# Kernel tuning notes

Hardware: AMD Instinct MI355X
Metric: run time of the kernel (lower is better)

Reference implementation:

```python
import jax, jax.numpy as jnp
import numpy as np

N = 30000      # total nodes across batch
E = 480000     # edges (before self-loops)
B = 48         # graphs in batch
H = 4          # heads
D = 64         # hidden per head
NIN = 8
NOUT = 128
L = 10
SLOPE = 0.2    # GATConv default negative_slope


def setup_inputs() -> dict:
    key = jax.random.key(0)
    ks = jax.random.split(key, 12)
    s = 0.05
    x = jax.random.normal(ks[0], (N, NIN), jnp.float32)
    edge_index = jax.random.randint(ks[1], (2, E), 0, N, dtype=jnp.int32)
    batch = jnp.sort(jax.random.randint(ks[2], (N,), 0, B, dtype=jnp.int32))
    # layer 0 params (input dim NIN)
    W0 = jax.random.normal(ks[3], (NIN, H * D), jnp.float32) * s
    a_src0 = jax.random.normal(ks[4], (H, D), jnp.float32) * s
    a_dst0 = jax.random.normal(ks[5], (H, D), jnp.float32) * s
    b0 = jnp.zeros((H * D,), jnp.float32)
    # layers 1..L-1 (input dim H*D)
    Ws = jax.random.normal(ks[6], (L - 1, H * D, H * D), jnp.float32) * s
    a_srcs = jax.random.normal(ks[7], (L - 1, H, D), jnp.float32) * s
    a_dsts = jax.random.normal(ks[8], (L - 1, H, D), jnp.float32) * s
    bs = jnp.zeros((L - 1, H * D), jnp.float32)
    # readout head: GELU -> Linear(4*H*D -> NOUT)
    head_W = jax.random.normal(ks[9], (4 * H * D, NOUT), jnp.float32) * s
    head_b = jnp.zeros((NOUT,), jnp.float32)
    return dict(x=x, edge_index=edge_index, batch=batch,
                W0=W0, a_src0=a_src0, a_dst0=a_dst0, b0=b0,
                Ws=Ws, a_srcs=a_srcs, a_dsts=a_dsts, bs=bs,
                head_W=head_W, head_b=head_b)


def _gat_layer(x, W, a_src, a_dst, b, src, dst):
    n = x.shape[0]
    h = (x @ W).reshape(n, H, D)                      # [N,H,D]
    alpha_src = jnp.einsum('nhd,hd->nh', h, a_src)    # [N,H]
    alpha_dst = jnp.einsum('nhd,hd->nh', h, a_dst)
    e = jax.nn.leaky_relu(alpha_src[src] + alpha_dst[dst], SLOPE)  # [Etot,H]
    # segment softmax over destination neighborhoods
    m = jax.ops.segment_max(e, dst, num_segments=n)
    e = jnp.exp(e - m[dst])
    z = jax.ops.segment_sum(e, dst, num_segments=n)
    alpha = e / (z[dst] + 1e-16)                      # [Etot,H]
    msg = h[src] * alpha[:, :, None]                  # [Etot,H,D]
    out = jax.ops.segment_sum(msg, dst, num_segments=n)
    return out.reshape(n, H * D) + b


def reference(x, edge_index, batch, W0, a_src0, a_dst0, b0,
              Ws, a_srcs, a_dsts, bs, head_W, head_b):
    # add self loops (GATConv default add_self_loops=True)
    loops = jnp.arange(N, dtype=edge_index.dtype)
    src = jnp.concatenate([edge_index[0], loops])
    dst = jnp.concatenate([edge_index[1], loops])

    h = _gat_layer(x, W0, a_src0, a_dst0, b0, src, dst)
    for i in range(L - 1):
        h = jax.nn.gelu(h, approximate=False)  # dropout = identity (eval)
        h = _gat_layer(h, Ws[i], a_srcs[i], a_dsts[i], bs[i], src, dst)

    # MultiAggregation([min, max, mean, sum]) over graphs
    cnt = jax.ops.segment_sum(jnp.ones((N,), h.dtype), batch, num_segments=B)
    g_sum = jax.ops.segment_sum(h, batch, num_segments=B)
    g_mean = g_sum / jnp.maximum(cnt, 1.0)[:, None]
    g_min = jax.ops.segment_min(h, batch, num_segments=B)
    g_max = jax.ops.segment_max(h, batch, num_segments=B)
    g = jnp.concatenate([g_min, g_max, g_mean, g_sum], axis=-1)  # [B, 4*H*D]

    return jax.nn.gelu(g, approximate=False) @ head_W + head_b   # [B, NOUT]
```

## Files before the change

kernel.cpp:

```cpp
#include <hip/hip_runtime.h>
#include <math.h>

#define NN   30000
#define EE   480000
#define ETOT 510000
#define BB   48
#define HHH  4
#define DDD  64
#define CCH  256
#define NINP 8
#define NOUTP 128
#define NLAY 10
#define SLOPE 0.2f
#define PCHUNK 32

typedef short v8s  __attribute__((ext_vector_type(8)));
typedef float v4f  __attribute__((ext_vector_type(4)));

__device__ __forceinline__ float gelu_f(float x){
    return 0.5f * x * (1.0f + erff(x * 0.70710678118654752f));
}
__device__ __forceinline__ unsigned short f2bf(float f){
    unsigned u = __float_as_uint(f);
    unsigned r = u + 0x7FFF + ((u >> 16) & 1);
    return (unsigned short)(r >> 16);
}
__device__ __forceinline__ float bf2f(unsigned short b){
    return __uint_as_float(((unsigned)b) << 16);
}
__device__ __forceinline__ float lrelu(float e){
    return (e > 0.f) ? e : SLOPE * e;
}
__device__ __forceinline__ unsigned pack2(float a, float b){
    return (unsigned)f2bf(a) | ((unsigned)f2bf(b) << 16);
}
__device__ __forceinline__ float4 up4(uint2 u){
    float4 r;
    r.x = __uint_as_float(u.x << 16);
    r.y = __uint_as_float(u.x & 0xFFFF0000u);
    r.z = __uint_as_float(u.y << 16);
    r.w = __uint_as_float(u.y & 0xFFFF0000u);
    return r;
}

__global__ void count_k(const int* __restrict__ ei, int* __restrict__ cnt){
    int e = blockIdx.x * 256 + threadIdx.x;
    if (e >= ETOT) return;
    int d = (e < EE) ? ei[EE + e] : (e - EE);
    atomicAdd(&cnt[d], 1);
}

__global__ __launch_bounds__(1024) void scan_k(const int* __restrict__ cnt, int* __restrict__ row_ptr){
    const int PER = 30;
    int t = threadIdx.x;
    int base = t * PER;
    int v[PER];
    int sum = 0;
#pragma unroll
    for (int i = 0; i < PER; ++i){
        int x = (base + i < NN) ? cnt[base + i] : 0;
        v[i] = sum;
        sum += x;
    }
    int lane = t & 63, w = t >> 6;
    int inc = sum;
#pragma unroll
    for (int off = 1; off < 64; off <<= 1){
        int u = __shfl_up(inc, off);
        if (lane >= off) inc += u;
    }
    __shared__ int wtot[16], woff[16];
    if (lane == 63) wtot[w] = inc;
    __syncthreads();
    if (t == 0){
        int r = 0;
        for (int i = 0; i < 16; ++i){ woff[i] = r; r += wtot[i]; }
        row_ptr[NN] = r;
    }
    __syncthreads();
    int excl = woff[w] + (inc - sum);
#pragma unroll
    for (int i = 0; i < PER; ++i){
        if (base + i < NN) row_ptr[base + i] = excl + v[i];
    }
}

__global__ void scatter_k(const int* __restrict__ ei, const int* __restrict__ row_ptr,
                          int* __restrict__ cursor, int* __restrict__ csr_src){
    int e = blockIdx.x * 256 + threadIdx.x;
    if (e >= ETOT) return;
    int s, d;
    if (e < EE){ s = ei[e]; d = ei[EE + e]; } else { s = d = e - EE; }
    int pos = row_ptr[d] + atomicAdd(&cursor[d], 1);
    csr_src[pos] = s;
}

__global__ __launch_bounds__(256) void wconv_k(const float* __restrict__ Ws,
                                               unsigned short* __restrict__ WT_hi,
                                               unsigned short* __restrict__ WT_lo){
    __shared__ float tile[32][33];
    int l = blockIdx.x;
    int kt = (blockIdx.y >> 3) * 32;
    int nt = (blockIdx.y & 7) * 32;
    const float* W = Ws + (size_t)l * CCH * CCH;
    unsigned short* th = WT_hi + (size_t)l * CCH * CCH;
    unsigned short* tl = WT_lo + (size_t)l * CCH * CCH;
    int tx = threadIdx.x & 31, ty = threadIdx.x >> 5;
#pragma unroll
    for (int r = ty; r < 32; r += 8)
        tile[r][tx] = W[(size_t)(kt + r) * CCH + nt + tx];
    __syncthreads();
#pragma unroll
    for (int r = ty; r < 32; r += 8){
        float w = tile[tx][r];
        unsigned short h = f2bf(w);
        size_t o = (size_t)(nt + r) * CCH + kt + tx;
        th[o] = h;
        tl[o] = f2bf(w - bf2f(h));
    }
}

__global__ __launch_bounds__(256) void waconv_k(const float* __restrict__ Ws,
                                                const float* __restrict__ a_srcs,
                                                const float* __restrict__ a_dsts,
                                                unsigned short* __restrict__ wa_hi,
                                                unsigned short* __restrict__ wa_lo){
    int l = blockIdx.x;
    int j = blockIdx.y;
    int k = threadIdx.x;
    const float* W = Ws + (size_t)l * CCH * CCH;
    const float* av = (j < 4) ? (a_srcs + (size_t)l * CCH + j * DDD)
                              : (a_dsts + (size_t)l * CCH + (j - 4) * DDD);
    int cb = (j & 3) * DDD;
    float s = 0.f;
    const float4* wp = (const float4*)(W + (size_t)k * CCH + cb);
    const float4* ap = (const float4*)av;
#pragma unroll
    for (int d = 0; d < DDD / 4; ++d){
        float4 wv = wp[d], avv = ap[d];
        s += wv.x * avv.x + wv.y * avv.y + wv.z * avv.z + wv.w * avv.w;
    }
    unsigned short hb = f2bf(s);
    wa_hi[((size_t)l * 16 + j) * CCH + k] = hb;
    wa_lo[((size_t)l * 16 + j) * CCH + k] = f2bf(s - bf2f(hb));
    if (j >= 4){
        wa_hi[((size_t)l * 16 + j + 4) * CCH + k] = 0;
        wa_lo[((size_t)l * 16 + j + 4) * CCH + k] = 0;
        wa_hi[((size_t)l * 16 + j + 8) * CCH + k] = 0;
        wa_lo[((size_t)l * 16 + j + 8) * CCH + k] = 0;
    }
}

__global__ __launch_bounds__(256) void l0_fused(const float* __restrict__ x,
                                                const float* __restrict__ W0,
                                                const float* __restrict__ a_src,
                                                const float* __restrict__ a_dst,
                                                unsigned short* __restrict__ hout,
                                                float* __restrict__ asb,
                                                float* __restrict__ adb){
    __shared__ float xs[NINP];
    int n = blockIdx.x;
    int c = threadIdx.x;
    if (c < NINP) xs[c] = x[n * NINP + c];
    __syncthreads();
    float acc = 0.f;
#pragma unroll
    for (int k = 0; k < NINP; ++k) acc += xs[k] * W0[k * CCH + c];
    hout[(size_t)n * CCH + c] = f2bf(acc);
    int hh = c >> 6, lane = c & 63;
    float s1 = acc * a_src[hh * DDD + lane];
    float s2 = acc * a_dst[hh * DDD + lane];
#pragma unroll
    for (int off = 32; off; off >>= 1){
        s1 += __shfl_xor(s1, off);
        s2 += __shfl_xor(s2, off);
    }
    if (lane == 0){
        asb[(size_t)n * HHH + hh] = s1;
        adb[(size_t)n * HHH + hh] = s2;
    }
}

__global__ __launch_bounds__(256) void gemm_mfma(const unsigned short* __restrict__ A,
                                                 const unsigned short* __restrict__ Bhi,
                                                 const unsigned short* __restrict__ Blo,
                                                 const unsigned short* __restrict__ WAhi,
                                                 const unsigned short* __restrict__ WAlo,
                                                 unsigned short* __restrict__ C,
                                                 float* __restrict__ asb,
                                                 float* __restrict__ adb){
    int tid  = threadIdx.x;
    int lane = tid & 63, wave = tid >> 6;
    int wr = wave >> 1, wc = wave & 1;
    int rowBase = blockIdx.y * 128 + wr * 64;
    int colBase = blockIdx.x * 128 + wc * 64;
    int fr = lane & 15;
    int kg = lane >> 4;
    bool doAlpha = (blockIdx.x == 0) && (wc == 0);

    v4f acc[4][4];
#pragma unroll
    for (int mi = 0; mi < 4; ++mi)
#pragma unroll
        for (int ni = 0; ni < 4; ++ni) acc[mi][ni] = (v4f){0.f, 0.f, 0.f, 0.f};
    v4f acca[4];
#pragma unroll
    for (int mi = 0; mi < 4; ++mi) acca[mi] = (v4f){0.f, 0.f, 0.f, 0.f};

    const unsigned short* aptr[4];
#pragma unroll
    for (int mi = 0; mi < 4; ++mi){
        int r = rowBase + mi * 16 + fr;
        if (r >= NN) r = NN - 1;
        aptr[mi] = A + (size_t)r * CCH + kg * 8;
    }
    const unsigned short* bhp[4];
    const unsigned short* blp[4];
#pragma unroll
    for (int ni = 0; ni < 4; ++ni){
        int c = colBase + ni * 16 + fr;
        bhp[ni] = Bhi + (size_t)c * CCH + kg * 8;
        blp[ni] = Blo + (size_t)c * CCH + kg * 8;
    }
    const unsigned short* wahp = WAhi + (size_t)fr * CCH + kg * 8;
    const unsigned short* walp = WAlo + (size_t)fr * CCH + kg * 8;

    for (int kc = 0; kc < CCH; kc += 32){
        v8s a[4], bh[4], bl[4];
#pragma unroll
        for (int mi = 0; mi < 4; ++mi) a[mi] = *(const v8s*)(aptr[mi] + kc);
#pragma unroll
        for (int ni = 0; ni < 4; ++ni){
            bh[ni] = *(const v8s*)(bhp[ni] + kc);
            bl[ni] = *(const v8s*)(blp[ni] + kc);
        }
#pragma unroll
        for (int mi = 0; mi < 4; ++mi)
#pragma unroll
            for (int ni = 0; ni < 4; ++ni){
                acc[mi][ni] = __builtin_amdgcn_mfma_f32_16x16x32_bf16(a[mi], bh[ni], acc[mi][ni], 0, 0, 0);
                acc[mi][ni] = __builtin_amdgcn_mfma_f32_16x16x32_bf16(a[mi], bl[ni], acc[mi][ni], 0, 0, 0);
            }
        if (doAlpha){
            v8s wh = *(const v8s*)(wahp + kc);
            v8s wl = *(const v8s*)(walp + kc);
#pragma unroll
            for (int mi = 0; mi < 4; ++mi){
                acca[mi] = __builtin_amdgcn_mfma_f32_16x16x32_bf16(a[mi], wh, acca[mi], 0, 0, 0);
                acca[mi] = __builtin_amdgcn_mfma_f32_16x16x32_bf16(a[mi], wl, acca[mi], 0, 0, 0);
            }
        }
    }

#pragma unroll
    for (int mi = 0; mi < 4; ++mi)
#pragma unroll
        for (int j = 0; j < 4; ++j){
            int r = rowBase + mi * 16 + kg * 4 + j;
            if (r < NN){
#pragma unroll
                for (int ni = 0; ni < 4; ++ni)
                    C[(size_t)r * CCH + colBase + ni * 16 + fr] = f2bf(acc[mi][ni][j]);
            }
        }
    if (doAlpha){
#pragma unroll
        for (int mi = 0; mi < 4; ++mi)
#pragma unroll
            for (int j = 0; j < 4; ++j){
                int r = rowBase + mi * 16 + kg * 4 + j;
                if (r < NN){
                    float val = acca[mi][j];
                    if (fr < 4)      asb[(size_t)r * HHH + fr]       = val;
                    else if (fr < 8) adb[(size_t)r * HHH + (fr - 4)] = val;
                }
            }
    }
}

#define LOADG8(gg, U0, U1, U2, U3, A0, A1, A2, A3)                     \
    { int _b = (gg) << 3;                                              \
      int _e0 = _b + half, _e1 = _b + 2 + half;                        \
      int _e2 = _b + 4 + half, _e3 = _b + 6 + half;                    \
      int _i0 = ix_w[_e0], _i1 = ix_w[_e1];                            \
      int _i2 = ix_w[_e2], _i3 = ix_w[_e3];                            \
      A0 = al_w[_e0 * HHH + hc8];                                      \
      A1 = al_w[_e1 * HHH + hc8];                                      \
      A2 = al_w[_e2 * HHH + hc8];                                      \
      A3 = al_w[_e3 * HHH + hc8];                                      \
      U0 = *(const uint4*)(h + (size_t)_i0 * CCH + coff8);             \
      U1 = *(const uint4*)(h + (size_t)_i1 * CCH + coff8);             \
      U2 = *(const uint4*)(h + (size_t)_i2 * CCH + coff8);             \
      U3 = *(const uint4*)(h + (size_t)_i3 * CCH + coff8); }

#define CONSUME8(U0, U1, U2, U3, A0, A1, A2, A3)                       \
    { float4 _l0 = up4(make_uint2(U0.x, U0.y)), _h0 = up4(make_uint2(U0.z, U0.w)); \
      float4 _l1 = up4(make_uint2(U1.x, U1.y)), _h1 = up4(make_uint2(U1.z, U1.w)); \
      float4 _l2 = up4(make_uint2(U2.x, U2.y)), _h2 = up4(make_uint2(U2.z, U2.w)); \
      float4 _l3 = up4(make_uint2(U3.x, U3.y)), _h3 = up4(make_uint2(U3.z, U3.w)); \
      accLo.x += _l0.x * A0 + _l1.x * A1 + _l2.x * A2 + _l3.x * A3;    \
      accLo.y += _l0.y * A0 + _l1.y * A1 + _l2.y * A2 + _l3.y * A3;    \
      accLo.z += _l0.z * A0 + _l1.z * A1 + _l2.z * A2 + _l3.z * A3;    \
      accLo.w += _l0.w * A0 + _l1.w * A1 + _l2.w * A2 + _l3.w * A3;    \
      accHi.x += _h0.x * A0 + _h1.x * A1 + _h2.x * A2 + _h3.x * A3;    \
      accHi.y += _h0.y * A0 + _h1.y * A1 + _h2.y * A2 + _h3.y * A3;    \
      accHi.z += _h0.z * A0 + _h1.z * A1 + _h2.z * A2 + _h3.z * A3;    \
      accHi.w += _h0.w * A0 + _h1.w * A1 + _h2.w * A2 + _h3.w * A3; }

__global__ __launch_bounds__(256) void agg_k(const unsigned short* __restrict__ h,
                                             const float* __restrict__ asrc,
                                             const float* __restrict__ adst,
                                             const float* __restrict__ bias,
                                             const int* __restrict__ row_ptr,
                                             const int* __restrict__ csr_src,
                                             unsigned short* __restrict__ outg,
                                             float* __restrict__ outf,
                                             int mode){
    __shared__ float s_al[4][64 * HHH];
    __shared__ int   s_ix[4][64];

    int wave = threadIdx.x >> 6, lane = threadIdx.x & 63;
    int n = blockIdx.x * 4 + wave;
    int row0 = row_ptr[n];
    int deg  = row_ptr[n + 1] - row0;
    float4 ad = *(const float4*)(adst + (size_t)n * HHH);
    float* al_w = s_al[wave];
    int*   ix_w = s_ix[wave];

    if (deg <= 64){
        int k = lane;
        int s = 0;
        float e0 = -INFINITY, e1 = -INFINITY, e2 = -INFINITY, e3 = -INFINITY;
        if (k < deg){
            s = csr_src[row0 + k];
            float4 as = *(const float4*)(asrc + (size_t)s * HHH);
            e0 = lrelu(as.x + ad.x); e1 = lrelu(as.y + ad.y);
            e2 = lrelu(as.z + ad.z); e3 = lrelu(as.w + ad.w);
        }
        float m0 = e0, m1 = e1, m2 = e2, m3 = e3;
#pragma unroll
        for (int off = 32; off; off >>= 1){
            m0 = fmaxf(m0, __shfl_xor(m0, off));
            m1 = fmaxf(m1, __shfl_xor(m1, off));
            m2 = fmaxf(m2, __shfl_xor(m2, off));
            m3 = fmaxf(m3, __shfl_xor(m3, off));
        }
        float x0 = 0.f, x1 = 0.f, x2 = 0.f, x3 = 0.f;
        if (k < deg){
            x0 = __expf(e0 - m0); x1 = __expf(e1 - m1);
            x2 = __expf(e2 - m2); x3 = __expf(e3 - m3);
        }
        float z0 = x0, z1 = x1, z2 = x2, z3 = x3;
#pragma unroll
        for (int off = 32; off; off >>= 1){
            z0 += __shfl_xor(z0, off);
            z1 += __shfl_xor(z1, off);
            z2 += __shfl_xor(z2, off);
            z3 += __shfl_xor(z3, off);
        }
        if (k < deg){
            float4 alv;
            alv.x = x0 / (z0 + 1e-16f);
            alv.y = x1 / (z1 + 1e-16f);
            alv.z = x2 / (z2 + 1e-16f);
            alv.w = x3 / (z3 + 1e-16f);
            ix_w[k] = s;
            *(float4*)&al_w[k * HHH] = alv;
        }
        int half  = lane >> 5;
        int l32   = lane & 31;
        int coff8 = l32 << 3;
        int hc8   = l32 >> 3;
        float4 accLo = make_float4(0.f, 0.f, 0.f, 0.f);
        float4 accHi = make_float4(0.f, 0.f, 0.f, 0.f);

        int ng = deg >> 3;
        uint4 uA0, uA1, uA2, uA3, uB0, uB1, uB2, uB3;
        float aA0, aA1, aA2, aA3, aB0, aB1, aB2, aB3;
        if (ng > 0) LOADG8(0, uA0, uA1, uA2, uA3, aA0, aA1, aA2, aA3);
        if (ng > 1) LOADG8(1, uB0, uB1, uB2, uB3, aB0, aB1, aB2, aB3);
        for (int g = 0; g < ng; g += 2){
            if (g + 2 < ng) {
                CONSUME8(uA0, uA1, uA2, uA3, aA0, aA1, aA2, aA3);
                LOADG8(g + 2, uA0, uA1, uA2, uA3, aA0, aA1, aA2, aA3);
            } else {
                CONSUME8(uA0, uA1, uA2, uA3, aA0, aA1, aA2, aA3);
            }
            if (g + 1 < ng){
                if (g + 3 < ng) {
                    CONSUME8(uB0, uB1, uB2, uB3, aB0, aB1, aB2, aB3);
                    LOADG8(g + 3, uB0, uB1, uB2, uB3, aB0, aB1, aB2, aB3);
                } else {
                    CONSUME8(uB0, uB1, uB2, uB3, aB0, aB1, aB2, aB3);
                }
            }
        }
        for (int kk = ng << 3; kk < deg; kk += 2){
            int e = kk + half;
            if (e < deg){
                int i0 = ix_w[e];
                float a0 = al_w[e * HHH + hc8];
                uint4 u = *(const uint4*)(h + (size_t)i0 * CCH + coff8);
                float4 lo = up4(make_uint2(u.x, u.y)), hi = up4(make_uint2(u.z, u.w));
                accLo.x += lo.x * a0; accLo.y += lo.y * a0;
                accLo.z += lo.z * a0; accLo.w += lo.w * a0;
                accHi.x += hi.x * a0; accHi.y += hi.y * a0;
                accHi.z += hi.z * a0; accHi.w += hi.w * a0;
            }
        }
        accLo.x += __shfl_xor(accLo.x, 32); accLo.y += __shfl_xor(accLo.y, 32);
        accLo.z += __shfl_xor(accLo.z, 32); accLo.w += __shfl_xor(accLo.w, 32);
        accHi.x += __shfl_xor(accHi.x, 32); accHi.y += __shfl_xor(accHi.y, 32);
        accHi.z += __shfl_xor(accHi.z, 32); accHi.w += __shfl_xor(accHi.w, 32);
        if (half == 0){
            float4 b0v = *(const float4*)(bias + coff8);
            float4 b1v = *(const float4*)(bias + coff8 + 4);
            accLo.x += b0v.x; accLo.y += b0v.y; accLo.z += b0v.z; accLo.w += b0v.w;
            accHi.x += b1v.x; accHi.y += b1v.y; accHi.z += b1v.z; accHi.w += b1v.w;
            if (mode == 0){
                uint4 o;
                o.x = pack2(gelu_f(accLo.x), gelu_f(accLo.y));
                o.y = pack2(gelu_f(accLo.z), gelu_f(accLo.w));
                o.z = pack2(gelu_f(accHi.x), gelu_f(accHi.y));
                o.w = pack2(gelu_f(accHi.z), gelu_f(accHi.w));
                *(uint4*)(outg + (size_t)n * CCH + coff8) = o;
            } else {
                *(float4*)(outf + (size_t)n * CCH + coff8)     = accLo;
                *(float4*)(outf + (size_t)n * CCH + coff8 + 4) = accHi;
            }
        }
        return;
    }

    int coff = lane << 2;
    int hc   = lane >> 4;
    float4 acc = make_float4(0.f, 0.f, 0.f, 0.f);
    float m0 = -INFINITY, m1 = -INFINITY, m2 = -INFINITY, m3 = -INFINITY;
    float z0 = 0.f, z1 = 0.f, z2 = 0.f, z3 = 0.f;
    for (int c0 = 0; c0 < deg; c0 += 64){
        int k = c0 + lane;
        float e0 = -INFINITY, e1 = -INFINITY, e2 = -INFINITY, e3 = -INFINITY;
        if (k < deg){
            int s = csr_src[row0 + k];
            float4 as = *(const float4*)(asrc + (size_t)s * HHH);
            e0 = lrelu(as.x + ad.x); e1 = lrelu(as.y + ad.y);
            e2 = lrelu(as.z + ad.z); e3 = lrelu(as.w + ad.w);
        }
        float c0m = e0, c1m = e1, c2m = e2, c3m = e3;
#pragma unroll
        for (int off = 32; off; off >>= 1){
            c0m = fmaxf(c0m, __shfl_xor(c0m, off));
            c1m = fmaxf(c1m, __shfl_xor(c1m, off));
            c2m = fmaxf(c2m, __shfl_xor(c2m, off));
            c3m = fmaxf(c3m, __shfl_xor(c3m, off));
        }
        float n0 = fmaxf(m0, c0m), n1 = fmaxf(m1, c1m);
        float n2 = fmaxf(m2, c2m), n3 = fmaxf(m3, c3m);
        float x0 = 0.f, x1 = 0.f, x2 = 0.f, x3 = 0.f;
        if (k < deg){
            x0 = __expf(e0 - n0); x1 = __expf(e1 - n1);
            x2 = __expf(e2 - n2); x3 = __expf(e3 - n3);
        }
        float s0 = x0, s1 = x1, s2 = x2, s3 = x3;
#pragma unroll
        for (int off = 32; off; off >>= 1){
            s0 += __shfl_xor(s0, off);
            s1 += __shfl_xor(s1, off);
            s2 += __shfl_xor(s2, off);
            s3 += __shfl_xor(s3, off);
        }
        z0 = z0 * ((m0 == -INFINITY) ? 0.f : __expf(m0 - n0)) + s0;
        z1 = z1 * ((m1 == -INFINITY) ? 0.f : __expf(m1 - n1)) + s1;
        z2 = z2 * ((m2 == -INFINITY) ? 0.f : __expf(m2 - n2)) + s2;
        z3 = z3 * ((m3 == -INFINITY) ? 0.f : __expf(m3 - n3)) + s3;
        m0 = n0; m1 = n1; m2 = n2; m3 = n3;
    }
    float iz0 = 1.f / (z0 + 1e-16f), iz1 = 1.f / (z1 + 1e-16f);
    float iz2 = 1.f / (z2 + 1e-16f), iz3 = 1.f / (z3 + 1e-16f);
    for (int c0 = 0; c0 < deg; c0 += 64){
        int k = c0 + lane;
        if (k < deg){
            int s = csr_src[row0 + k];
            float4 as = *(const float4*)(asrc + (size_t)s * HHH);
            float4 alv;
            alv.x = __expf(lrelu(as.x + ad.x) - m0) * iz0;
            alv.y = __expf(lrelu(as.y + ad.y) - m1) * iz1;
            alv.z = __expf(lrelu(as.z + ad.z) - m2) * iz2;
            alv.w = __expf(lrelu(as.w + ad.w) - m3) * iz3;
            ix_w[lane] = s;
            *(float4*)&al_w[lane * HHH] = alv;
        }
        int cnt = deg - c0; if (cnt > 64) cnt = 64;
        for (int j = 0; j < cnt; ++j){
            int i0 = ix_w[j];
            float a0 = al_w[j * HHH + hc];
            float4 v0 = up4(*(const uint2*)(h + (size_t)i0 * CCH + coff));
            acc.x += v0.x * a0; acc.y += v0.y * a0; acc.z += v0.z * a0; acc.w += v0.w * a0;
        }
    }
    float4 bv = *(const float4*)(bias + coff);
    acc.x += bv.x; acc.y += bv.y; acc.z += bv.z; acc.w += bv.w;
    if (mode == 0){
        uint2 o;
        o.x = pack2(gelu_f(acc.x), gelu_f(acc.y));
        o.y = pack2(gelu_f(acc.z), gelu_f(acc.w));
        *(uint2*)(outg + (size_t)n * CCH + coff) = o;
    } else {
        *(float4*)(outf + (size_t)n * CCH + coff) = acc;
    }
}

__global__ void gptr_k(const int* __restrict__ batch, int* __restrict__ gptr){
    int i = blockIdx.x * 256 + threadIdx.x;
    if (i >= NN) return;
    int bi = batch[i];
    int bp = (i == 0) ? -1 : batch[i - 1];
    for (int g = bp + 1; g <= bi; ++g) gptr[g] = i;
    if (i == NN - 1){
        for (int g = bi + 1; g <= BB; ++g) gptr[g] = NN;
    }
}

__global__ __launch_bounds__(256) void pool1_k(const float* __restrict__ h,
                                               const int* __restrict__ gptr,
                                               float* __restrict__ part){
    const int S1 = BB * PCHUNK * CCH;
    int b = blockIdx.x, j = blockIdx.y, c = threadIdx.x;
    int s = gptr[b], e = gptr[b + 1];
    int len = e - s;
    int per = (len + PCHUNK - 1) / PCHUNK;
    int r0 = s + j * per;
    int r1 = r0 + per; if (r1 > e) r1 = e;
    float mn = INFINITY, mx = -INFINITY, sm = 0.f;
    int n = r0;
    for (; n + 4 <= r1; n += 4){
        float v0 = h[(size_t)(n + 0) * CCH + c];
        float v1 = h[(size_t)(n + 1) * CCH + c];
        float v2 = h[(size_t)(n + 2) * CCH + c];
        float v3 = h[(size_t)(n + 3) * CCH + c];
        mn = fminf(mn, fminf(fminf(v0, v1), fminf(v2, v3)));
        mx = fmaxf(mx, fmaxf(fmaxf(v0, v1), fmaxf(v2, v3)));
        sm += (v0 + v1) + (v2 + v3);
    }
    for (; n < r1; ++n){
        float v = h[(size_t)n * CCH + c];
        mn = fminf(mn, v); mx = fmaxf(mx, v); sm += v;
    }
    size_t o = ((size_t)b * PCHUNK + j) * CCH + c;
    part[o] = mn; part[S1 + o] = mx; part[2 * (size_t)S1 + o] = sm;
}

__global__ __launch_bounds__(256) void pool2_k(const float* __restrict__ part,
                                               const int* __restrict__ gptr,
                                               float* __restrict__ gbuf){
    const int S1 = BB * PCHUNK * CCH;
    int b = blockIdx.x, c = threadIdx.x;
    float mn = INFINITY, mx = -INFINITY, sm = 0.f;
#pragma unroll
    for (int j = 0; j < PCHUNK; ++j){
        size_t o = ((size_t)b * PCHUNK + j) * CCH + c;
        mn = fminf(mn, part[o]);
        mx = fmaxf(mx, part[S1 + o]);
        sm += part[2 * (size_t)S1 + o];
    }
    int cnt = gptr[b + 1] - gptr[b];
    float mean = sm / fmaxf((float)cnt, 1.0f);
    if (cnt == 0){ mn = 0.f; mx = 0.f; }
    gbuf[b * 4 * CCH + 0 * CCH + c] = mn;
    gbuf[b * 4 * CCH + 1 * CCH + c] = mx;
    gbuf[b * 4 * CCH + 2 * CCH + c] = mean;
    gbuf[b * 4 * CCH + 3 * CCH + c] = sm;
}

__global__ __launch_bounds__(128) void head_k(const float* __restrict__ gbuf,
                                              const float* __restrict__ head_W,
                                              const float* __restrict__ head_b,
                                              float* __restrict__ out){
    __shared__ float gs[4 * CCH];
    int b = blockIdx.x;
    int o = threadIdx.x;
    for (int k = o; k < 4 * CCH; k += 128) gs[k] = gelu_f(gbuf[b * 4 * CCH + k]);
    __syncthreads();
    float acc = head_b[o];
    for (int k = 0; k < 4 * CCH; ++k) acc += gs[k] * head_W[k * NOUTP + o];
    out[b * NOUTP + o] = acc;
}

extern "C" void kernel_launch(void* const* d_in, const int* in_sizes, int n_in,
                              void* d_out, int out_size, void* d_ws, size_t ws_size,
                              hipStream_t stream){
    const float* x        = (const float*)d_in[0];
    const int*   ei       = (const int*)  d_in[1];
    const int*   batch    = (const int*)  d_in[2];
    const float* W0       = (const float*)d_in[3];
    const float* a_src0   = (const float*)d_in[4];
    const float* a_dst0   = (const float*)d_in[5];
    const float* b0       = (const float*)d_in[6];
    const float* Ws       = (const float*)d_in[7];
    const float* a_srcs   = (const float*)d_in[8];
    const float* a_dsts   = (const float*)d_in[9];
    const float* bs       = (const float*)d_in[10];
    const float* head_W   = (const float*)d_in[11];
    const float* head_b   = (const float*)d_in[12];
    float* out = (float*)d_out;

    char* p = (char*)d_ws;
    float* buf0f = (float*)p;                   p += (size_t)NN * CCH * 4;
    unsigned short* buf0g = (unsigned short*)p; p += (size_t)NN * CCH * 2;
    unsigned short* buf1  = (unsigned short*)p; p += (size_t)NN * CCH * 2;
    float* asb  = (float*)p;                   p += (size_t)NN * HHH * 4;
    float* adb  = (float*)p;                   p += (size_t)NN * HHH * 4;
    int* row_ptr = (int*)p;                    p += 120016;
    int* cnt     = (int*)p;                    p += (size_t)NN * 4;
    int* csr_src = (int*)p;                    p += (size_t)ETOT * 4;
    float* gbuf  = (float*)p;                  p += (size_t)BB * 4 * CCH * 4;
    int* gptr    = (int*)p;                    p += 208;
    unsigned short* wthi = (unsigned short*)p; p += (size_t)(NLAY - 1) * CCH * CCH * 2;
    unsigned short* wtlo = (unsigned short*)p; p += (size_t)(NLAY - 1) * CCH * CCH * 2;
    unsigned short* wahi = (unsigned short*)p; p += (size_t)(NLAY - 1) * 16 * CCH * 2;
    unsigned short* walo = (unsigned short*)p; p += (size_t)(NLAY - 1) * 16 * CCH * 2;
    float* pscr = (float*)p;                   p += (size_t)3 * BB * PCHUNK * CCH * 4;

    hipMemsetAsync(cnt, 0, (size_t)NN * 4, stream);
    count_k<<<(ETOT + 255) / 256, 256, 0, stream>>>(ei, cnt);
    scan_k<<<1, 1024, 0, stream>>>(cnt, row_ptr);
    hipMemsetAsync(cnt, 0, (size_t)NN * 4, stream);
    scatter_k<<<(ETOT + 255) / 256, 256, 0, stream>>>(ei, row_ptr, cnt, csr_src);
    gptr_k<<<(NN + 255) / 256, 256, 0, stream>>>(batch, gptr);
    wconv_k<<<dim3(NLAY - 1, 64), 256, 0, stream>>>(Ws, wthi, wtlo);
    waconv_k<<<dim3(NLAY - 1, 8), 256, 0, stream>>>(Ws, a_srcs, a_dsts, wahi, walo);

    l0_fused<<<NN, 256, 0, stream>>>(x, W0, a_src0, a_dst0, buf1, asb, adb);
    agg_k<<<NN / 4, 256, 0, stream>>>(buf1, asb, adb, b0, row_ptr, csr_src,
                                      buf0g, buf0f, 0);

    dim3 ggrid(2, (NN + 127) / 128);
    for (int l = 1; l < NLAY; ++l){
        const unsigned short* whl = wthi + (size_t)(l - 1) * CCH * CCH;
        const unsigned short* wll = wtlo + (size_t)(l - 1) * CCH * CCH;
        const unsigned short* wal_h = wahi + (size_t)(l - 1) * 16 * CCH;
        const unsigned short* wal_l = walo + (size_t)(l - 1) * 16 * CCH;
        const float* bl  = bs + (size_t)(l - 1) * CCH;
        gemm_mfma<<<ggrid, 256, 0, stream>>>(buf0g, whl, wll, wal_h, wal_l, buf1, asb, adb);
        agg_k<<<NN / 4, 256, 0, stream>>>(buf1, asb, adb, bl, row_ptr, csr_src,
                                          buf0g, buf0f, (l == NLAY - 1) ? 1 : 0);
    }

    dim3 pgrid(BB, PCHUNK);
    pool1_k<<<pgrid, 256, 0, stream>>>(buf0f, gptr, pscr);
    pool2_k<<<BB, 256, 0, stream>>>(pscr, gptr, gbuf);
    head_k<<<BB, 128, 0, stream>>>(gbuf, head_W, head_b, out);
}
```

Measured before the change: 979.6 us.

## Aggregate two destination nodes per wave and drop softmax max subtraction

Each wave of the aggregation kernel now processes two destination nodes. It issues the first neighbour-row gathers for both nodes before consuming either, so more independent global loads are in flight to hide gather latency, and the grid is halved accordingly. The segment-softmax max reduction is removed: logits are exponentiated directly, which saves one cross-lane reduction per head. In exchange it risks overflow or precision loss if attention logits become large. If either node has degree above 64, both fall back to the generic per-node path.

```diff
diff --git a/kernel.cpp b/kernel.cpp
--- a/kernel.cpp
+++ b/kernel.cpp
@@ -278,160 +278,14 @@
     }
 }
 
-#define LOADG8(gg, U0, U1, U2, U3, A0, A1, A2, A3)                     \
-    { int _b = (gg) << 3;                                              \
-      int _e0 = _b + half, _e1 = _b + 2 + half;                        \
-      int _e2 = _b + 4 + half, _e3 = _b + 6 + half;                    \
-      int _i0 = ix_w[_e0], _i1 = ix_w[_e1];                            \
-      int _i2 = ix_w[_e2], _i3 = ix_w[_e3];                            \
-      A0 = al_w[_e0 * HHH + hc8];                                      \
-      A1 = al_w[_e1 * HHH + hc8];                                      \
-      A2 = al_w[_e2 * HHH + hc8];                                      \
-      A3 = al_w[_e3 * HHH + hc8];                                      \
-      U0 = *(const uint4*)(h + (size_t)_i0 * CCH + coff8);             \
-      U1 = *(const uint4*)(h + (size_t)_i1 * CCH + coff8);             \
-      U2 = *(const uint4*)(h + (size_t)_i2 * CCH + coff8);             \
-      U3 = *(const uint4*)(h + (size_t)_i3 * CCH + coff8); }
-
-#define CONSUME8(U0, U1, U2, U3, A0, A1, A2, A3)                       \
-    { float4 _l0 = up4(make_uint2(U0.x, U0.y)), _h0 = up4(make_uint2(U0.z, U0.w)); \
-      float4 _l1 = up4(make_uint2(U1.x, U1.y)), _h1 = up4(make_uint2(U1.z, U1.w)); \
-      float4 _l2 = up4(make_uint2(U2.x, U2.y)), _h2 = up4(make_uint2(U2.z, U2.w)); \
-      float4 _l3 = up4(make_uint2(U3.x, U3.y)), _h3 = up4(make_uint2(U3.z, U3.w)); \
-      accLo.x += _l0.x * A0 + _l1.x * A1 + _l2.x * A2 + _l3.x * A3;    \
-      accLo.y += _l0.y * A0 + _l1.y * A1 + _l2.y * A2 + _l3.y * A3;    \
-      accLo.z += _l0.z * A0 + _l1.z * A1 + _l2.z * A2 + _l3.z * A3;    \
-      accLo.w += _l0.w * A0 + _l1.w * A1 + _l2.w * A2 + _l3.w * A3;    \
-      accHi.x += _h0.x * A0 + _h1.x * A1 + _h2.x * A2 + _h3.x * A3;    \
-      accHi.y += _h0.y * A0 + _h1.y * A1 + _h2.y * A2 + _h3.y * A3;    \
-      accHi.z += _h0.z * A0 + _h1.z * A1 + _h2.z * A2 + _h3.z * A3;    \
-      accHi.w += _h0.w * A0 + _h1.w * A1 + _h2.w * A2 + _h3.w * A3; }
-
-__global__ __launch_bounds__(256) void agg_k(const unsigned short* __restrict__ h,
-                                             const float* __restrict__ asrc,
-                                             const float* __restrict__ adst,
-                                             const float* __restrict__ bias,
-                                             const int* __restrict__ row_ptr,
-                                             const int* __restrict__ csr_src,
-                                             unsigned short* __restrict__ outg,
-                                             float* __restrict__ outf,
-                                             int mode){
-    __shared__ float s_al[4][64 * HHH];
-    __shared__ int   s_ix[4][64];
-
-    int wave = threadIdx.x >> 6, lane = threadIdx.x & 63;
-    int n = blockIdx.x * 4 + wave;
-    int row0 = row_ptr[n];
-    int deg  = row_ptr[n + 1] - row0;
-    float4 ad = *(const float4*)(adst + (size_t)n * HHH);
-    float* al_w = s_al[wave];
-    int*   ix_w = s_ix[wave];
-
-    if (deg <= 64){
-        int k = lane;
-        int s = 0;
-        float e0 = -INFINITY, e1 = -INFINITY, e2 = -INFINITY, e3 = -INFINITY;
-        if (k < deg){
-            s = csr_src[row0 + k];
-            float4 as = *(const float4*)(asrc + (size_t)s * HHH);
-            e0 = lrelu(as.x + ad.x); e1 = lrelu(as.y + ad.y);
-            e2 = lrelu(as.z + ad.z); e3 = lrelu(as.w + ad.w);
-        }
-        float m0 = e0, m1 = e1, m2 = e2, m3 = e3;
-#pragma unroll
-        for (int off = 32; off; off >>= 1){
-            m0 = fmaxf(m0, __shfl_xor(m0, off));
-            m1 = fmaxf(m1, __shfl_xor(m1, off));
-            m2 = fmaxf(m2, __shfl_xor(m2, off));
-            m3 = fmaxf(m3, __shfl_xor(m3, off));
-        }
-        float x0 = 0.f, x1 = 0.f, x2 = 0.f, x3 = 0.f;
-        if (k < deg){
-            x0 = __expf(e0 - m0); x1 = __expf(e1 - m1);
-            x2 = __expf(e2 - m2); x3 = __expf(e3 - m3);
-        }
-        float z0 = x0, z1 = x1, z2 = x2, z3 = x3;
-#pragma unroll
-        for (int off = 32; off; off >>= 1){
-            z0 += __shfl_xor(z0, off);
-            z1 += __shfl_xor(z1, off);
-            z2 += __shfl_xor(z2, off);
-            z3 += __shfl_xor(z3, off);
-        }
-        if (k < deg){
-            float4 alv;
-            alv.x = x0 / (z0 + 1e-16f);
-            alv.y = x1 / (z1 + 1e-16f);
-            alv.z = x2 / (z2 + 1e-16f);
-            alv.w = x3 / (z3 + 1e-16f);
-            ix_w[k] = s;
-            *(float4*)&al_w[k * HHH] = alv;
-        }
-        int half  = lane >> 5;
-        int l32   = lane & 31;
-        int coff8 = l32 << 3;
-        int hc8   = l32 >> 3;
-        float4 accLo = make_float4(0.f, 0.f, 0.f, 0.f);
-        float4 accHi = make_float4(0.f, 0.f, 0.f, 0.f);
-
-        int ng = deg >> 3;
-        uint4 uA0, uA1, uA2, uA3, uB0, uB1, uB2, uB3;
-        float aA0, aA1, aA2, aA3, aB0, aB1, aB2, aB3;
-        if (ng > 0) LOADG8(0, uA0, uA1, uA2, uA3, aA0, aA1, aA2, aA3);
-        if (ng > 1) LOADG8(1, uB0, uB1, uB2, uB3, aB0, aB1, aB2, aB3);
-        for (int g = 0; g < ng; g += 2){
-            if (g + 2 < ng) {
-                CONSUME8(uA0, uA1, uA2, uA3, aA0, aA1, aA2, aA3);
-                LOADG8(g + 2, uA0, uA1, uA2, uA3, aA0, aA1, aA2, aA3);
-            } else {
-                CONSUME8(uA0, uA1, uA2, uA3, aA0, aA1, aA2, aA3);
-            }
-            if (g + 1 < ng){
-                if (g + 3 < ng) {
-                    CONSUME8(uB0, uB1, uB2, uB3, aB0, aB1, aB2, aB3);
-                    LOADG8(g + 3, uB0, uB1, uB2, uB3, aB0, aB1, aB2, aB3);
-                } else {
-                    CONSUME8(uB0, uB1, uB2, uB3, aB0, aB1, aB2, aB3);
-                }
-            }
-        }
-        for (int kk = ng << 3; kk < deg; kk += 2){
-            int e = kk + half;
-            if (e < deg){
-                int i0 = ix_w[e];
-                float a0 = al_w[e * HHH + hc8];
-                uint4 u = *(const uint4*)(h + (size_t)i0 * CCH + coff8);
-                float4 lo = up4(make_uint2(u.x, u.y)), hi = up4(make_uint2(u.z, u.w));
-                accLo.x += lo.x * a0; accLo.y += lo.y * a0;
-                accLo.z += lo.z * a0; accLo.w += lo.w * a0;
-                accHi.x += hi.x * a0; accHi.y += hi.y * a0;
-                accHi.z += hi.z * a0; accHi.w += hi.w * a0;
-            }
-        }
-        accLo.x += __shfl_xor(accLo.x, 32); accLo.y += __shfl_xor(accLo.y, 32);
-        accLo.z += __shfl_xor(accLo.z, 32); accLo.w += __shfl_xor(accLo.w, 32);
-        accHi.x += __shfl_xor(accHi.x, 32); accHi.y += __shfl_xor(accHi.y, 32);
-        accHi.z += __shfl_xor(accHi.z, 32); accHi.w += __shfl_xor(accHi.w, 32);
-        if (half == 0){
-            float4 b0v = *(const float4*)(bias + coff8);
-            float4 b1v = *(const float4*)(bias + coff8 + 4);
-            accLo.x += b0v.x; accLo.y += b0v.y; accLo.z += b0v.z; accLo.w += b0v.w;
-            accHi.x += b1v.x; accHi.y += b1v.y; accHi.z += b1v.z; accHi.w += b1v.w;
-            if (mode == 0){
-                uint4 o;
-                o.x = pack2(gelu_f(accLo.x), gelu_f(accLo.y));
-                o.y = pack2(gelu_f(accLo.z), gelu_f(accLo.w));
-                o.z = pack2(gelu_f(accHi.x), gelu_f(accHi.y));
-                o.w = pack2(gelu_f(accHi.z), gelu_f(accHi.w));
-                *(uint4*)(outg + (size_t)n * CCH + coff8) = o;
-            } else {
-                *(float4*)(outf + (size_t)n * CCH + coff8)     = accLo;
-                *(float4*)(outf + (size_t)n * CCH + coff8 + 4) = accHi;
-            }
-        }
-        return;
-    }
-
+__device__ void agg_node_generic(const unsigned short* __restrict__ h,
+                                 const float* __restrict__ asrc,
+                                 const float* __restrict__ bias,
+                                 const int* __restrict__ csr_src,
+                                 unsigned short* __restrict__ outg,
+                                 float* __restrict__ outf,
+                                 int mode, int n, int row0, int deg,
+                                 float4 ad, float* al_w, int* ix_w, int lane){
     int coff = lane << 2;
     int hc   = lane >> 4;
     float4 acc = make_float4(0.f, 0.f, 0.f, 0.f);
@@ -508,6 +362,207 @@
     } else {
         *(float4*)(outf + (size_t)n * CCH + coff) = acc;
     }
+}
+
+#define LOADG8X(ixp, alp, gg, U0, U1, U2, U3, A0, A1, A2, A3)          \
+    { int _b = (gg) << 3;                                              \
+      int _e0 = _b + half, _e1 = _b + 2 + half;                        \
+      int _e2 = _b + 4 + half, _e3 = _b + 6 + half;                    \
+      int _i0 = ixp[_e0], _i1 = ixp[_e1];                              \
+      int _i2 = ixp[_e2], _i3 = ixp[_e3];                              \
+      A0 = alp[_e0 * HHH + hc8];                                       \
+      A1 = alp[_e1 * HHH + hc8];                                       \
+      A2 = alp[_e2 * HHH + hc8];                                       \
+      A3 = alp[_e3 * HHH + hc8];                                       \
+      U0 = *(const uint4*)(h + (size_t)_i0 * CCH + coff8);             \
+      U1 = *(const uint4*)(h + (size_t)_i1 * CCH + coff8);             \
+      U2 = *(const uint4*)(h + (size_t)_i2 * CCH + coff8);             \
+      U3 = *(const uint4*)(h + (size_t)_i3 * CCH + coff8); }
+
+#define CONSUME8X(U0, U1, U2, U3, A0, A1, A2, A3, ALO, AHI)            \
+    { float4 _l0 = up4(make_uint2(U0.x, U0.y)), _h0 = up4(make_uint2(U0.z, U0.w)); \
+      float4 _l1 = up4(make_uint2(U1.x, U1.y)), _h1 = up4(make_uint2(U1.z, U1.w)); \
+      float4 _l2 = up4(make_uint2(U2.x, U2.y)), _h2 = up4(make_uint2(U2.z, U2.w)); \
+      float4 _l3 = up4(make_uint2(U3.x, U3.y)), _h3 = up4(make_uint2(U3.z, U3.w)); \
+      ALO.x += _l0.x * A0 + _l1.x * A1 + _l2.x * A2 + _l3.x * A3;      \
+      ALO.y += _l0.y * A0 + _l1.y * A1 + _l2.y * A2 + _l3.y * A3;      \
+      ALO.z += _l0.z * A0 + _l1.z * A1 + _l2.z * A2 + _l3.z * A3;      \
+      ALO.w += _l0.w * A0 + _l1.w * A1 + _l2.w * A2 + _l3.w * A3;      \
+      AHI.x += _h0.x * A0 + _h1.x * A1 + _h2.x * A2 + _h3.x * A3;      \
+      AHI.y += _h0.y * A0 + _h1.y * A1 + _h2.y * A2 + _h3.y * A3;      \
+      AHI.z += _h0.z * A0 + _h1.z * A1 + _h2.z * A2 + _h3.z * A3;      \
+      AHI.w += _h0.w * A0 + _h1.w * A1 + _h2.w * A2 + _h3.w * A3; }
+
+#define STOREOUT(nn, ALO, AHI)                                         \
+    { ALO.x += __shfl_xor(ALO.x, 32); ALO.y += __shfl_xor(ALO.y, 32);  \
+      ALO.z += __shfl_xor(ALO.z, 32); ALO.w += __shfl_xor(ALO.w, 32);  \
+      AHI.x += __shfl_xor(AHI.x, 32); AHI.y += __shfl_xor(AHI.y, 32);  \
+      AHI.z += __shfl_xor(AHI.z, 32); AHI.w += __shfl_xor(AHI.w, 32);  \
+      if (half == 0){                                                  \
+          float4 _b0 = *(const float4*)(bias + coff8);                 \
+          float4 _b1 = *(const float4*)(bias + coff8 + 4);             \
+          ALO.x += _b0.x; ALO.y += _b0.y; ALO.z += _b0.z; ALO.w += _b0.w; \
+          AHI.x += _b1.x; AHI.y += _b1.y; AHI.z += _b1.z; AHI.w += _b1.w; \
+          if (mode == 0){                                              \
+              uint4 _o;                                                \
+              _o.x = pack2(gelu_f(ALO.x), gelu_f(ALO.y));              \
+              _o.y = pack2(gelu_f(ALO.z), gelu_f(ALO.w));              \
+              _o.z = pack2(gelu_f(AHI.x), gelu_f(AHI.y));              \
+              _o.w = pack2(gelu_f(AHI.z), gelu_f(AHI.w));              \
+              *(uint4*)(outg + (size_t)(nn) * CCH + coff8) = _o;       \
+          } else {                                                     \
+              *(float4*)(outf + (size_t)(nn) * CCH + coff8)     = ALO; \
+              *(float4*)(outf + (size_t)(nn) * CCH + coff8 + 4) = AHI; \
+          }                                                            \
+      } }
+
+__global__ __launch_bounds__(256) void agg_k(const unsigned short* __restrict__ h,
+                                             const float* __restrict__ asrc,
+                                             const float* __restrict__ adst,
+                                             const float* __restrict__ bias,
+                                             const int* __restrict__ row_ptr,
+                                             const int* __restrict__ csr_src,
+                                             unsigned short* __restrict__ outg,
+                                             float* __restrict__ outf,
+                                             int mode){
+    __shared__ float s_al[8][64 * HHH];
+    __shared__ int   s_ix[8][64];
+
+    int wave = threadIdx.x >> 6, lane = threadIdx.x & 63;
+    int nA = blockIdx.x * 8 + wave * 2;
+    int nB = nA + 1;
+    int r0 = row_ptr[nA], r1 = row_ptr[nA + 1], r2 = row_ptr[nB + 1];
+    int degA = r1 - r0, degB = r2 - r1;
+    float4 adA = *(const float4*)(adst + (size_t)nA * HHH);
+    float4 adB = *(const float4*)(adst + (size_t)nB * HHH);
+    float* alA = s_al[wave * 2];     int* ixA = s_ix[wave * 2];
+    float* alB = s_al[wave * 2 + 1]; int* ixB = s_ix[wave * 2 + 1];
+
+    if (degA > 64 || degB > 64){
+        agg_node_generic(h, asrc, bias, csr_src, outg, outf, mode, nA, r0, degA, adA, alA, ixA, lane);
+        agg_node_generic(h, asrc, bias, csr_src, outg, outf, mode, nB, r1, degB, adB, alB, ixB, lane);
+        return;
+    }
+
+    int sA = 0, sB = 0;
+    float xA0 = 0.f, xA1 = 0.f, xA2 = 0.f, xA3 = 0.f;
+    float xB0 = 0.f, xB1 = 0.f, xB2 = 0.f, xB3 = 0.f;
+    if (lane < degA){
+        sA = csr_src[r0 + lane];
+        float4 as = *(const float4*)(asrc + (size_t)sA * HHH);
+        xA0 = __expf(lrelu(as.x + adA.x)); xA1 = __expf(lrelu(as.y + adA.y));
+        xA2 = __expf(lrelu(as.z + adA.z)); xA3 = __expf(lrelu(as.w + adA.w));
+    }
+    if (lane < degB){
+        sB = csr_src[r1 + lane];
+        float4 as = *(const float4*)(asrc + (size_t)sB * HHH);
+        xB0 = __expf(lrelu(as.x + adB.x)); xB1 = __expf(lrelu(as.y + adB.y));
+        xB2 = __expf(lrelu(as.z + adB.z)); xB3 = __expf(lrelu(as.w + adB.w));
+    }
+    float zA0 = xA0, zA1 = xA1, zA2 = xA2, zA3 = xA3;
+    float zB0 = xB0, zB1 = xB1, zB2 = xB2, zB3 = xB3;
+#pragma unroll
+    for (int off = 32; off; off >>= 1){
+        zA0 += __shfl_xor(zA0, off); zA1 += __shfl_xor(zA1, off);
+        zA2 += __shfl_xor(zA2, off); zA3 += __shfl_xor(zA3, off);
+        zB0 += __shfl_xor(zB0, off); zB1 += __shfl_xor(zB1, off);
+        zB2 += __shfl_xor(zB2, off); zB3 += __shfl_xor(zB3, off);
+    }
+    if (lane < degA){
+        float4 alv;
+        alv.x = xA0 / (zA0 + 1e-16f); alv.y = xA1 / (zA1 + 1e-16f);
+        alv.z = xA2 / (zA2 + 1e-16f); alv.w = xA3 / (zA3 + 1e-16f);
+        ixA[lane] = sA;
+        *(float4*)&alA[lane * HHH] = alv;
+    }
+    if (lane < degB){
+        float4 alv;
+        alv.x = xB0 / (zB0 + 1e-16f); alv.y = xB1 / (zB1 + 1e-16f);
+        alv.z = xB2 / (zB2 + 1e-16f); alv.w = xB3 / (zB3 + 1e-16f);
+        ixB[lane] = sB;
+        *(float4*)&alB[lane * HHH] = alv;
+    }
+
+    int half  = lane >> 5;
+    int l32   = lane & 31;
+    int coff8 = l32 << 3;
+    int hc8   = l32 >> 3;
+    float4 accLoA = make_float4(0.f,0.f,0.f,0.f), accHiA = make_float4(0.f,0.f,0.f,0.f);
+    float4 accLoB = make_float4(0.f,0.f,0.f,0.f), accHiB = make_float4(0.f,0.f,0.f,0.f);
+    int ngA = degA >> 3, ngB = degB >> 3;
+
+    uint4 uA0,uA1,uA2,uA3, uA4,uA5,uA6,uA7;
+    uint4 uB0,uB1,uB2,uB3, uB4,uB5,uB6,uB7;
+    float aA0,aA1,aA2,aA3, aA4,aA5,aA6,aA7;
+    float aB0,aB1,aB2,aB3, aB4,aB5,aB6,aB7;
+
+    if (ngA > 0) LOADG8X(ixA, alA, 0, uA0,uA1,uA2,uA3, aA0,aA1,aA2,aA3);
+    if (ngB > 0) LOADG8X(ixB, alB, 0, uB0,uB1,uB2,uB3, aB0,aB1,aB2,aB3);
+    if (ngA > 1) LOADG8X(ixA, alA, 1, uA4,uA5,uA6,uA7, aA4,aA5,aA6,aA7);
+    if (ngB > 1) LOADG8X(ixB, alB, 1, uB4,uB5,uB6,uB7, aB4,aB5,aB6,aB7);
+
+    for (int g = 0; g < ngA; g += 2){
+        if (g + 2 < ngA){
+            CONSUME8X(uA0,uA1,uA2,uA3, aA0,aA1,aA2,aA3, accLoA, accHiA);
+            LOADG8X(ixA, alA, g + 2, uA0,uA1,uA2,uA3, aA0,aA1,aA2,aA3);
+        } else {
+            CONSUME8X(uA0,uA1,uA2,uA3, aA0,aA1,aA2,aA3, accLoA, accHiA);
+        }
+        if (g + 1 < ngA){
+            if (g + 3 < ngA){
+                CONSUME8X(uA4,uA5,uA6,uA7, aA4,aA5,aA6,aA7, accLoA, accHiA);
+                LOADG8X(ixA, alA, g + 3, uA4,uA5,uA6,uA7, aA4,aA5,aA6,aA7);
+            } else {
+                CONSUME8X(uA4,uA5,uA6,uA7, aA4,aA5,aA6,aA7, accLoA, accHiA);
+            }
+        }
+    }
+    for (int kk = ngA << 3; kk < degA; kk += 2){
+        int e = kk + half;
+        if (e < degA){
+            int i0 = ixA[e];
+            float a0 = alA[e * HHH + hc8];
+            uint4 u = *(const uint4*)(h + (size_t)i0 * CCH + coff8);
+            float4 lo = up4(make_uint2(u.x, u.y)), hi = up4(make_uint2(u.z, u.w));
+            accLoA.x += lo.x * a0; accLoA.y += lo.y * a0;
+            accLoA.z += lo.z * a0; accLoA.w += lo.w * a0;
+            accHiA.x += hi.x * a0; accHiA.y += hi.y * a0;
+            accHiA.z += hi.z * a0; accHiA.w += hi.w * a0;
+        }
+    }
+
+    for (int g = 0; g < ngB; g += 2){
+        if (g + 2 < ngB){
+            CONSUME8X(uB0,uB1,uB2,uB3, aB0,aB1,aB2,aB3, accLoB, accHiB);
+            LOADG8X(ixB, alB, g + 2, uB0,uB1,uB2,uB3, aB0,aB1,aB2,aB3);
+        } else {
+            CONSUME8X(uB0,uB1,uB2,uB3, aB0,aB1,aB2,aB3, accLoB, accHiB);
+        }
+        if (g + 1 < ngB){
+            if (g + 3 < ngB){
+                CONSUME8X(uB4,uB5,uB6,uB7, aB4,aB5,aB6,aB7, accLoB, accHiB);
+                LOADG8X(ixB, alB, g + 3, uB4,uB5,uB6,uB7, aB4,aB5,aB6,aB7);
+            } else {
+                CONSUME8X(uB4,uB5,uB6,uB7, aB4,aB5,aB6,aB7, accLoB, accHiB);
+            }
+        }
+    }
+    for (int kk = ngB << 3; kk < degB; kk += 2){
+        int e = kk + half;
+        if (e < degB){
+            int i0 = ixB[e];
+            float a0 = alB[e * HHH + hc8];
+            uint4 u = *(const uint4*)(h + (size_t)i0 * CCH + coff8);
+            float4 lo = up4(make_uint2(u.x, u.y)), hi = up4(make_uint2(u.z, u.w));
+            accLoB.x += lo.x * a0; accLoB.y += lo.y * a0;
+            accLoB.z += lo.z * a0; accLoB.w += lo.w * a0;
+            accHiB.x += hi.x * a0; accHiB.y += hi.y * a0;
+            accHiB.z += hi.z * a0; accHiB.w += hi.w * a0;
+        }
+    }
+
+    STOREOUT(nA, accLoA, accHiA);
+    STOREOUT(nB, accLoB, accHiB);
 }
 
 __global__ void gptr_k(const int* __restrict__ batch, int* __restrict__ gptr){
@@ -631,7 +686,7 @@
     waconv_k<<<dim3(NLAY - 1, 8), 256, 0, stream>>>(Ws, a_srcs, a_dsts, wahi, walo);
 
     l0_fused<<<NN, 256, 0, stream>>>(x, W0, a_src0, a_dst0, buf1, asb, adb);
-    agg_k<<<NN / 4, 256, 0, stream>>>(buf1, asb, adb, b0, row_ptr, csr_src,
+    agg_k<<<NN / 8, 256, 0, stream>>>(buf1, asb, adb, b0, row_ptr, csr_src,
                                       buf0g, buf0f, 0);
 
     dim3 ggrid(2, (NN + 127) / 128);
@@ -642,7 +697,7 @@
         const unsigned short* wal_l = walo + (size_t)(l - 1) * 16 * CCH;
         const float* bl  = bs + (size_t)(l - 1) * CCH;
         gemm_mfma<<<ggrid, 256, 0, stream>>>(buf0g, whl, wll, wal_h, wal_l, buf1, asb, adb);
-        agg_k<<<NN / 4, 256, 0, stream>>>(buf1, asb, adb, bl, row_ptr, csr_src,
+        agg_k<<<NN / 8, 256, 0, stream>>>(buf1, asb, adb, bl, row_ptr, csr_src,
                                           buf0g, buf0f, (l == NLAY - 1) ? 1 : 0);
     }
 
```

New measurement: 1.014 ms. +3.5%, slower.
